# Kernel tuning notes

Hardware: AMD Instinct MI355X
Metric: run time of the kernel (lower is better)

Reference implementation:

```python
import jax, jax.numpy as jnp
import numpy as np

N_NODES = 50000


def gcn_conv(x, src, dst, W, b, n_nodes):
    """PyG-style GCNConv: linear transform, then symmetric-normalized
    aggregation with self-loops added."""
    # add self loops
    loop = jnp.arange(n_nodes, dtype=src.dtype)
    src_l = jnp.concatenate([src, loop])
    dst_l = jnp.concatenate([dst, loop])
    # degree (of dst, including self loops) and symmetric norm
    deg = jax.ops.segment_sum(jnp.ones_like(dst_l, dtype=x.dtype), dst_l,
                              num_segments=n_nodes)
    dinv = jnp.where(deg > 0, jax.lax.rsqrt(deg), 0.0)
    norm = dinv[src_l] * dinv[dst_l]  # [E+N]
    h = x @ W  # [N, out]
    msg = norm[:, None] * h[src_l]  # [E+N, out]
    out = jax.ops.segment_sum(msg, dst_l, num_segments=n_nodes)
    return out + b


def setup_inputs() -> dict:
    key = jax.random.key(0)
    k1, k2, k3, k4 = jax.random.split(key, 4)
    x = jax.random.normal(k1, (N_NODES, 512), dtype=jnp.float32)
    edge_index = jax.random.randint(k2, (2, 800000), 0, N_NODES, dtype=jnp.int32)
    W1 = jax.random.normal(k3, (512, 128), dtype=jnp.float32) * (1.0 / np.sqrt(512))
    b1 = jnp.zeros((128,), dtype=jnp.float32)
    W2 = jax.random.normal(k4, (128, 3), dtype=jnp.float32) * (1.0 / np.sqrt(128))
    b2 = jnp.zeros((3,), dtype=jnp.float32)
    return {"x": x, "edge_index": edge_index, "W1": W1, "b1": b1, "W2": W2, "b2": b2}


def reference(x, edge_index, W1, b1, W2, b2):
    src, dst = edge_index[0], edge_index[1]
    n = x.shape[0]
    h = gcn_conv(x, src, dst, W1, b1, n)
    h = jax.nn.relu(h)
    # dropout is identity in eval mode (training=False)
    out = gcn_conv(h, src, dst, W2, b2, n)
    return out
```

## Files before the change

### kernel.cpp

```cpp
#include <hip/hip_runtime.h>
#include <stdint.h>

#define N_NODES 50000
#define N_EDGES 800000
#define F_IN    512
#define F_HID   128
#define F_OUT   3
#define NBLK_SCAN 196
#define GEMM_BLOCKS 782
#define HIST_BLOCKS 3125
#define FILL_BLOCKS 3125
#define SCALE_BLOCKS 3125

typedef __attribute__((ext_vector_type(8))) short short8;
typedef __attribute__((ext_vector_type(4))) float f32x4;

__device__ __forceinline__ unsigned short f2bf(float f) {
  union { float f; unsigned u; } v; v.f = f;
  unsigned r = v.u + 0x7FFFu + ((v.u >> 16) & 1u);
  return (unsigned short)(r >> 16);
}

__device__ __forceinline__ short8 pack8(float4 a, float4 b) {
  short8 r;
  r[0] = (short)f2bf(a.x); r[1] = (short)f2bf(a.y);
  r[2] = (short)f2bf(a.z); r[3] = (short)f2bf(a.w);
  r[4] = (short)f2bf(b.x); r[5] = (short)f2bf(b.y);
  r[6] = (short)f2bf(b.z); r[7] = (short)f2bf(b.w);
  return r;
}

__device__ __forceinline__ unsigned scale2(unsigned u, float dd) {
  float lo = __uint_as_float(u << 16) * dd;
  float hi = __uint_as_float(u & 0xFFFF0000u) * dd;
  return (unsigned)f2bf(lo) | ((unsigned)f2bf(hi) << 16);
}

__device__ __forceinline__ void g2l16(const void* gsrc, void* ldst) {
  __builtin_amdgcn_global_load_lds(
      (const __attribute__((address_space(1))) unsigned int*)gsrc,
      (__attribute__((address_space(3))) unsigned int*)ldst, 16, 0, 0);
}

__global__ __launch_bounds__(256) void k_prep(const float* __restrict__ W1,
                                              unsigned short* __restrict__ W1t,
                                              int* __restrict__ count) {
  int idx = blockIdx.x * 256 + threadIdx.x;
  if (idx < N_NODES) count[idx] = 0;
  if (idx < F_IN * F_HID) {
    int k = idx >> 7;
    int n = idx & 127;
    W1t[n * F_IN + k] = f2bf(W1[idx]);
  }
}

__global__ __launch_bounds__(256) void k_gemm1_hist(const float* __restrict__ x,
                                                    const unsigned short* __restrict__ W1t,
                                                    unsigned short* __restrict__ h1b,
                                                    const int* __restrict__ dst,
                                                    int* __restrict__ count,
                                                    int* __restrict__ rank) {
  __shared__ float4 AsV[1024];
  __shared__ float4 BsV[1024];
  const int t = threadIdx.x;

  if (blockIdx.x >= GEMM_BLOCKS) {
    int e = (blockIdx.x - GEMM_BLOCKS) * 256 + t;
    if (e < N_EDGES) rank[e] = atomicAdd(&count[dst[e]], 1);
    return;
  }

  char* AsB = (char*)AsV;
  char* BsB = (char*)BsV;
  const int lane = t & 63;
  const int wid = t >> 6;
  const int lane15 = lane & 15;
  const int kgrp = (lane >> 4) << 3;
  const int row0 = blockIdx.x * 64;
  const int wrow = wid << 4;

  f32x4 acc[8];
  #pragma unroll
  for (int j = 0; j < 8; ++j) acc[j] = (f32x4)0.0f;

  for (int kt = 0; kt < 8; ++kt) {
    const int k0 = kt << 6;
    #pragma unroll
    for (int r = 0; r < 4; ++r) {
      const int i = (wid << 2) + r;
      const int o = (i << 10) + (lane << 4);
      {
        const int rowA = o >> 8;
        const int cb = (o & 255) ^ ((rowA & 7) << 4);
        int grow = row0 + rowA;
        grow = grow < N_NODES ? grow : N_NODES - 1;
        g2l16((const char*)x + (size_t)grow * 2048 + (k0 << 2) + cb,
              AsB + (i << 10));
      }
      {
        const int nB = o >> 7;
        const int kb = (o & 127) ^ ((nB & 7) << 4);
        g2l16((const char*)W1t + (size_t)nB * 1024 + (k0 << 1) + kb,
              BsB + (i << 10));
      }
    }
    __syncthreads();
    #pragma unroll
    for (int ks = 0; ks < 2; ++ks) {
      const int kk = (ks << 5) + kgrp;
      const int rowL = wrow + lane15;
      const int swA = (rowL & 7) << 4;
      const float4 xa = *reinterpret_cast<const float4*>(AsB + rowL * 256 + (((kk << 2)) ^ swA));
      const float4 xb = *reinterpret_cast<const float4*>(AsB + rowL * 256 + (((kk << 2) + 16) ^ swA));
      const short8 a = pack8(xa, xb);
      #pragma unroll
      for (int nr = 0; nr < 8; ++nr) {
        const int n = (nr << 4) + lane15;
        const short8 b = *reinterpret_cast<const short8*>(BsB + n * 128 + (((kk << 1)) ^ ((n & 7) << 4)));
        acc[nr] = __builtin_amdgcn_mfma_f32_16x16x32_bf16(a, b, acc[nr], 0, 0, 0);
      }
    }
    __syncthreads();
  }

  const int rgrp = (lane >> 4) << 2;
  const int rowb = row0 + wrow + rgrp;
  #pragma unroll
  for (int nr = 0; nr < 8; ++nr) {
    const int col = (nr << 4) + lane15;
    #pragma unroll
    for (int r = 0; r < 4; ++r) {
      const int row = rowb + r;
      if (row < N_NODES)
        h1b[(size_t)row * F_HID + col] = f2bf(acc[nr][r]);
    }
  }
}

__global__ __launch_bounds__(256) void k_scan1(const int* __restrict__ count,
                                               int* __restrict__ local_pre,
                                               int* __restrict__ blocksum) {
  __shared__ int s[256];
  int t = threadIdx.x;
  int i = blockIdx.x * 256 + t;
  int v = (i < N_NODES) ? count[i] : 0;
  s[t] = v;
  __syncthreads();
  #pragma unroll
  for (int off = 1; off < 256; off <<= 1) {
    int u = (t >= off) ? s[t - off] : 0;
    __syncthreads();
    s[t] += u;
    __syncthreads();
  }
  if (i < N_NODES) local_pre[i] = s[t] - v;
  if (t == 255) blocksum[blockIdx.x] = s[255];
}

__global__ __launch_bounds__(256) void k_scan3(const int* __restrict__ count,
                                               const int* __restrict__ local_pre,
                                               const int* __restrict__ blocksum,
                                               int* __restrict__ row_ptr,
                                               float* __restrict__ dinv) {
  __shared__ int s[256];
  __shared__ int blockoff;
  int t = threadIdx.x;
  int v = (t < NBLK_SCAN) ? blocksum[t] : 0;
  s[t] = v;
  __syncthreads();
  #pragma unroll
  for (int off = 1; off < 256; off <<= 1) {
    int u = (t >= off) ? s[t - off] : 0;
    __syncthreads();
    s[t] += u;
    __syncthreads();
  }
  if (t == blockIdx.x) blockoff = s[t] - v;
  __syncthreads();
  int i = blockIdx.x * 256 + t;
  if (i < N_NODES) {
    row_ptr[i] = local_pre[i] + blockoff;
    dinv[i] = rsqrtf((float)(count[i] + 1));
  }
  if (i == 0) row_ptr[N_NODES] = N_EDGES;
}

__global__ __launch_bounds__(256) void k_fill_scale(const int* __restrict__ src,
                                                    const int* __restrict__ dst,
                                                    const int* __restrict__ row_ptr,
                                                    const int* __restrict__ rank,
                                                    int* __restrict__ csr_src,
                                                    const float* __restrict__ dinv,
                                                    unsigned short* __restrict__ h1b) {
  int t = threadIdx.x;
  if (blockIdx.x < FILL_BLOCKS) {
    int e = blockIdx.x * 256 + t;
    if (e < N_EDGES) {
      int pos = row_ptr[dst[e]] + rank[e];
      csr_src[pos] = src[e];
    }
    return;
  }
  int gid = (blockIdx.x - FILL_BLOCKS) * 256 + t;
  int row = gid >> 4;
  float dd = dinv[row];
  uint4* p = reinterpret_cast<uint4*>(h1b) + gid;
  uint4 v = *p;
  v.x = scale2(v.x, dd);
  v.y = scale2(v.y, dd);
  v.z = scale2(v.z, dd);
  v.w = scale2(v.w, dd);
  *p = v;
}

__global__ __launch_bounds__(256) void k_agg1_fused(const int* __restrict__ row_ptr,
                                                    const int* __restrict__ csr_src,
                                                    const float* __restrict__ dinv,
                                                    const unsigned short* __restrict__ h1b,
                                                    const float* __restrict__ b1,
                                                    const float* __restrict__ W2,
                                                    float* __restrict__ t2p) {
  int t = threadIdx.x;
  int lane = t & 63;
  int node = blockIdx.x * 4 + (t >> 6);
  int g = lane >> 5;
  int fl = (lane & 31) << 2;
  float dd = dinv[node];
  f32x4 acc = (f32x4)0.0f;
  if (g == 0) {
    const uint2 sv = *reinterpret_cast<const uint2*>(h1b + (size_t)node * F_HID + fl);
    acc[0] = __uint_as_float(sv.x << 16);
    acc[1] = __uint_as_float(sv.x & 0xFFFF0000u);
    acc[2] = __uint_as_float(sv.y << 16);
    acc[3] = __uint_as_float(sv.y & 0xFFFF0000u);
  }
  int start = row_ptr[node], end = row_ptr[node + 1];
  int i = start + g;
  for (; i + 6 < end; i += 8) {
    int s0 = csr_src[i];
    int s1 = csr_src[i + 2];
    int s2 = csr_src[i + 4];
    int s3 = csr_src[i + 6];
    const uint2 v0 = *reinterpret_cast<const uint2*>(h1b + (size_t)s0 * F_HID + fl);
    const uint2 v1 = *reinterpret_cast<const uint2*>(h1b + (size_t)s1 * F_HID + fl);
    const uint2 v2 = *reinterpret_cast<const uint2*>(h1b + (size_t)s2 * F_HID + fl);
    const uint2 v3 = *reinterpret_cast<const uint2*>(h1b + (size_t)s3 * F_HID + fl);
    acc[0] += __uint_as_float(v0.x << 16);
    acc[1] += __uint_as_float(v0.x & 0xFFFF0000u);
    acc[2] += __uint_as_float(v0.y << 16);
    acc[3] += __uint_as_float(v0.y & 0xFFFF0000u);
    acc[0] += __uint_as_float(v1.x << 16);
    acc[1] += __uint_as_float(v1.x & 0xFFFF0000u);
    acc[2] += __uint_as_float(v1.y << 16);
    acc[3] += __uint_as_float(v1.y & 0xFFFF0000u);
    acc[0] += __uint_as_float(v2.x << 16);
    acc[1] += __uint_as_float(v2.x & 0xFFFF0000u);
    acc[2] += __uint_as_float(v2.y << 16);
    acc[3] += __uint_as_float(v2.y & 0xFFFF0000u);
    acc[0] += __uint_as_float(v3.x << 16);
    acc[1] += __uint_as_float(v3.x & 0xFFFF0000u);
    acc[2] += __uint_as_float(v3.y << 16);
    acc[3] += __uint_as_float(v3.y & 0xFFFF0000u);
  }
  for (; i < end; i += 2) {
    int s = csr_src[i];
    const uint2 v = *reinterpret_cast<const uint2*>(h1b + (size_t)s * F_HID + fl);
    acc[0] += __uint_as_float(v.x << 16);
    acc[1] += __uint_as_float(v.x & 0xFFFF0000u);
    acc[2] += __uint_as_float(v.y << 16);
    acc[3] += __uint_as_float(v.y & 0xFFFF0000u);
  }
  #pragma unroll
  for (int j = 0; j < 4; ++j) {
    float o = __shfl(acc[j], (lane & 31) + 32);
    acc[j] += o;
  }
  const float4 bb = *reinterpret_cast<const float4*>(b1 + fl);
  float v0 = fmaxf(fmaf(dd, acc[0], bb.x), 0.0f);
  float v1 = fmaxf(fmaf(dd, acc[1], bb.y), 0.0f);
  float v2 = fmaxf(fmaf(dd, acc[2], bb.z), 0.0f);
  float v3 = fmaxf(fmaf(dd, acc[3], bb.w), 0.0f);
  const float* w2r = W2 + fl * 3;
  float pr[3];
  #pragma unroll
  for (int c = 0; c < 3; ++c) {
    float p = v0 * w2r[c] + v1 * w2r[3 + c] + v2 * w2r[6 + c] + v3 * w2r[9 + c];
    p += __shfl_down(p, 16);
    p += __shfl_down(p, 8);
    p += __shfl_down(p, 4);
    p += __shfl_down(p, 2);
    p += __shfl_down(p, 1);
    pr[c] = p;
  }
  if (lane == 0) {
    float4 o;
    o.x = dd * pr[0]; o.y = dd * pr[1]; o.z = dd * pr[2]; o.w = 0.0f;
    *reinterpret_cast<float4*>(t2p + (size_t)node * 4) = o;
  }
}

__global__ __launch_bounds__(256) void k_agg2(const int* __restrict__ row_ptr,
                                              const int* __restrict__ csr_src,
                                              const float* __restrict__ dinv,
                                              const float* __restrict__ t2p,
                                              const float* __restrict__ b2,
                                              float* __restrict__ out) {
  int t = threadIdx.x;
  int node = blockIdx.x * 16 + (t >> 4);
  if (node >= N_NODES) return;
  int sl = t & 15;
  float a0 = 0.f, a1 = 0.f, a2 = 0.f;
  int start = row_ptr[node], end = row_ptr[node + 1];
  for (int i = start + sl; i < end; i += 16) {
    int s = csr_src[i];
    const float4 v = *reinterpret_cast<const float4*>(t2p + (size_t)s * 4);
    a0 += v.x; a1 += v.y; a2 += v.z;
  }
  #pragma unroll
  for (int off = 8; off > 0; off >>= 1) {
    a0 += __shfl_down(a0, off);
    a1 += __shfl_down(a1, off);
    a2 += __shfl_down(a2, off);
  }
  if (sl == 0) {
    float dd = dinv[node];
    const float4 sv = *reinterpret_cast<const float4*>(t2p + (size_t)node * 4);
    out[node * 3 + 0] = fmaf(dd, sv.x + a0, b2[0]);
    out[node * 3 + 1] = fmaf(dd, sv.y + a1, b2[1]);
    out[node * 3 + 2] = fmaf(dd, sv.z + a2, b2[2]);
  }
}

extern "C" void kernel_launch(void* const* d_in, const int* in_sizes, int n_in,
                              void* d_out, int out_size, void* d_ws, size_t ws_size,
                              hipStream_t stream) {
  const float* x  = (const float*)d_in[0];
  const int*   ei = (const int*)d_in[1];
  const float* W1 = (const float*)d_in[2];
  const float* b1 = (const float*)d_in[3];
  const float* W2 = (const float*)d_in[4];
  const float* b2 = (const float*)d_in[5];
  const int* src = ei;
  const int* dst = ei + N_EDGES;
  float* out = (float*)d_out;

  char* ws = (char*)d_ws;
  float*          dinv    = (float*)(ws + 0);
  int*            count   = (int*)  (ws + 200704);
  int*            rank    = (int*)  (ws + 401408);
  int*            row_ptr = (int*)  (ws + 3601408);
  int*            csr_src = (int*)  (ws + 3801600);
  unsigned short* W1t     = (unsigned short*)(ws + 7001600);
  float*          t2p     = (float*)(ws + 7132672);
  int*            local_pre = (int*)(ws + 7933440);
  int*            blocksum  = (int*)(ws + 8133440);
  unsigned short* h1b     = (unsigned short*)(ws + 8134656);

  k_prep      <<<256, 256, 0, stream>>>(W1, W1t, count);
  k_gemm1_hist<<<GEMM_BLOCKS + HIST_BLOCKS, 256, 0, stream>>>(x, W1t, h1b, dst, count, rank);
  k_scan1     <<<NBLK_SCAN, 256, 0, stream>>>(count, local_pre, blocksum);
  k_scan3     <<<NBLK_SCAN, 256, 0, stream>>>(count, local_pre, blocksum, row_ptr, dinv);
  k_fill_scale<<<FILL_BLOCKS + SCALE_BLOCKS, 256, 0, stream>>>(src, dst, row_ptr, rank, csr_src, dinv, h1b);
  k_agg1_fused<<<N_NODES / 4, 256, 0, stream>>>(row_ptr, csr_src, dinv, h1b, b1, W2, t2p);
  k_agg2      <<<(N_NODES + 15) / 16, 256, 0, stream>>>(row_ptr, csr_src, dinv, t2p, b2, out);
}
```

Measured before the change: 119.2 us.

## Move GEMM after degree scan and fold dinv scaling into its epilogue

Reorders the pipeline so the histogram runs alongside the W1 transpose, the scans run next, and the layer-1 GEMM runs afterward with the dinv row scaling applied in its epilogue. The CSR fill now shares a launch with the GEMM. This removes the separate read-modify-write pass over h1b. The count zeroing moves to a memset. The histogram no longer overlaps the GEMM, so the critical path changes.

```diff
diff --git a/kernel.cpp b/kernel.cpp
--- a/kernel.cpp
+++ b/kernel.cpp
@@ -7,10 +7,10 @@
 #define F_HID   128
 #define F_OUT   3
 #define NBLK_SCAN 196
+#define PREP_BLOCKS 256
+#define HIST_BLOCKS 3125
 #define GEMM_BLOCKS 782
-#define HIST_BLOCKS 3125
 #define FILL_BLOCKS 3125
-#define SCALE_BLOCKS 3125
 
 typedef __attribute__((ext_vector_type(8))) short short8;
 typedef __attribute__((ext_vector_type(4))) float f32x4;
@@ -30,43 +30,96 @@
   return r;
 }
 
-__device__ __forceinline__ unsigned scale2(unsigned u, float dd) {
-  float lo = __uint_as_float(u << 16) * dd;
-  float hi = __uint_as_float(u & 0xFFFF0000u) * dd;
-  return (unsigned)f2bf(lo) | ((unsigned)f2bf(hi) << 16);
-}
-
 __device__ __forceinline__ void g2l16(const void* gsrc, void* ldst) {
   __builtin_amdgcn_global_load_lds(
       (const __attribute__((address_space(1))) unsigned int*)gsrc,
       (__attribute__((address_space(3))) unsigned int*)ldst, 16, 0, 0);
 }
 
-__global__ __launch_bounds__(256) void k_prep(const float* __restrict__ W1,
-                                              unsigned short* __restrict__ W1t,
-                                              int* __restrict__ count) {
-  int idx = blockIdx.x * 256 + threadIdx.x;
-  if (idx < N_NODES) count[idx] = 0;
-  if (idx < F_IN * F_HID) {
+__global__ __launch_bounds__(256) void k_prep_hist(const float* __restrict__ W1,
+                                                   unsigned short* __restrict__ W1t,
+                                                   const int* __restrict__ dst,
+                                                   int* __restrict__ count,
+                                                   int* __restrict__ rank) {
+  int t = threadIdx.x;
+  if (blockIdx.x < PREP_BLOCKS) {
+    int idx = blockIdx.x * 256 + t;
     int k = idx >> 7;
     int n = idx & 127;
     W1t[n * F_IN + k] = f2bf(W1[idx]);
-  }
-}
-
-__global__ __launch_bounds__(256) void k_gemm1_hist(const float* __restrict__ x,
+    return;
+  }
+  int e = (blockIdx.x - PREP_BLOCKS) * 256 + t;
+  if (e < N_EDGES) rank[e] = atomicAdd(&count[dst[e]], 1);
+}
+
+__global__ __launch_bounds__(256) void k_scan1(const int* __restrict__ count,
+                                               int* __restrict__ local_pre,
+                                               int* __restrict__ blocksum) {
+  __shared__ int s[256];
+  int t = threadIdx.x;
+  int i = blockIdx.x * 256 + t;
+  int v = (i < N_NODES) ? count[i] : 0;
+  s[t] = v;
+  __syncthreads();
+  #pragma unroll
+  for (int off = 1; off < 256; off <<= 1) {
+    int u = (t >= off) ? s[t - off] : 0;
+    __syncthreads();
+    s[t] += u;
+    __syncthreads();
+  }
+  if (i < N_NODES) local_pre[i] = s[t] - v;
+  if (t == 255) blocksum[blockIdx.x] = s[255];
+}
+
+__global__ __launch_bounds__(256) void k_scan3(const int* __restrict__ count,
+                                               const int* __restrict__ local_pre,
+                                               const int* __restrict__ blocksum,
+                                               int* __restrict__ row_ptr,
+                                               float* __restrict__ dinv) {
+  __shared__ int s[256];
+  __shared__ int blockoff;
+  int t = threadIdx.x;
+  int v = (t < NBLK_SCAN) ? blocksum[t] : 0;
+  s[t] = v;
+  __syncthreads();
+  #pragma unroll
+  for (int off = 1; off < 256; off <<= 1) {
+    int u = (t >= off) ? s[t - off] : 0;
+    __syncthreads();
+    s[t] += u;
+    __syncthreads();
+  }
+  if (t == blockIdx.x) blockoff = s[t] - v;
+  __syncthreads();
+  int i = blockIdx.x * 256 + t;
+  if (i < N_NODES) {
+    row_ptr[i] = local_pre[i] + blockoff;
+    dinv[i] = rsqrtf((float)(count[i] + 1));
+  }
+  if (i == 0) row_ptr[N_NODES] = N_EDGES;
+}
+
+__global__ __launch_bounds__(256) void k_gemm1_fill(const float* __restrict__ x,
                                                     const unsigned short* __restrict__ W1t,
+                                                    const float* __restrict__ dinv,
                                                     unsigned short* __restrict__ h1b,
+                                                    const int* __restrict__ src,
                                                     const int* __restrict__ dst,
-                                                    int* __restrict__ count,
-                                                    int* __restrict__ rank) {
+                                                    const int* __restrict__ row_ptr,
+                                                    const int* __restrict__ rank,
+                                                    int* __restrict__ csr_src) {
   __shared__ float4 AsV[1024];
   __shared__ float4 BsV[1024];
   const int t = threadIdx.x;
 
   if (blockIdx.x >= GEMM_BLOCKS) {
     int e = (blockIdx.x - GEMM_BLOCKS) * 256 + t;
-    if (e < N_EDGES) rank[e] = atomicAdd(&count[dst[e]], 1);
+    if (e < N_EDGES) {
+      int pos = row_ptr[dst[e]] + rank[e];
+      csr_src[pos] = src[e];
+    }
     return;
   }
 
@@ -132,85 +185,9 @@
     for (int r = 0; r < 4; ++r) {
       const int row = rowb + r;
       if (row < N_NODES)
-        h1b[(size_t)row * F_HID + col] = f2bf(acc[nr][r]);
+        h1b[(size_t)row * F_HID + col] = f2bf(dinv[row] * acc[nr][r]);
     }
   }
-}
-
-__global__ __launch_bounds__(256) void k_scan1(const int* __restrict__ count,
-                                               int* __restrict__ local_pre,
-                                               int* __restrict__ blocksum) {
-  __shared__ int s[256];
-  int t = threadIdx.x;
-  int i = blockIdx.x * 256 + t;
-  int v = (i < N_NODES) ? count[i] : 0;
-  s[t] = v;
-  __syncthreads();
-  #pragma unroll
-  for (int off = 1; off < 256; off <<= 1) {
-    int u = (t >= off) ? s[t - off] : 0;
-    __syncthreads();
-    s[t] += u;
-    __syncthreads();
-  }
-  if (i < N_NODES) local_pre[i] = s[t] - v;
-  if (t == 255) blocksum[blockIdx.x] = s[255];
-}
-
-__global__ __launch_bounds__(256) void k_scan3(const int* __restrict__ count,
-                                               const int* __restrict__ local_pre,
-                                               const int* __restrict__ blocksum,
-                                               int* __restrict__ row_ptr,
-                                               float* __restrict__ dinv) {
-  __shared__ int s[256];
-  __shared__ int blockoff;
-  int t = threadIdx.x;
-  int v = (t < NBLK_SCAN) ? blocksum[t] : 0;
-  s[t] = v;
-  __syncthreads();
-  #pragma unroll
-  for (int off = 1; off < 256; off <<= 1) {
-    int u = (t >= off) ? s[t - off] : 0;
-    __syncthreads();
-    s[t] += u;
-    __syncthreads();
-  }
-  if (t == blockIdx.x) blockoff = s[t] - v;
-  __syncthreads();
-  int i = blockIdx.x * 256 + t;
-  if (i < N_NODES) {
-    row_ptr[i] = local_pre[i] + blockoff;
-    dinv[i] = rsqrtf((float)(count[i] + 1));
-  }
-  if (i == 0) row_ptr[N_NODES] = N_EDGES;
-}
-
-__global__ __launch_bounds__(256) void k_fill_scale(const int* __restrict__ src,
-                                                    const int* __restrict__ dst,
-                                                    const int* __restrict__ row_ptr,
-                                                    const int* __restrict__ rank,
-                                                    int* __restrict__ csr_src,
-                                                    const float* __restrict__ dinv,
-                                                    unsigned short* __restrict__ h1b) {
-  int t = threadIdx.x;
-  if (blockIdx.x < FILL_BLOCKS) {
-    int e = blockIdx.x * 256 + t;
-    if (e < N_EDGES) {
-      int pos = row_ptr[dst[e]] + rank[e];
-      csr_src[pos] = src[e];
-    }
-    return;
-  }
-  int gid = (blockIdx.x - FILL_BLOCKS) * 256 + t;
-  int row = gid >> 4;
-  float dd = dinv[row];
-  uint4* p = reinterpret_cast<uint4*>(h1b) + gid;
-  uint4 v = *p;
-  v.x = scale2(v.x, dd);
-  v.y = scale2(v.y, dd);
-  v.z = scale2(v.z, dd);
-  v.w = scale2(v.w, dd);
-  *p = v;
 }
 
 __global__ __launch_bounds__(256) void k_agg1_fused(const int* __restrict__ row_ptr,
@@ -356,11 +333,12 @@
   int*            blocksum  = (int*)(ws + 8133440);
   unsigned short* h1b     = (unsigned short*)(ws + 8134656);
 
-  k_prep      <<<256, 256, 0, stream>>>(W1, W1t, count);
-  k_gemm1_hist<<<GEMM_BLOCKS + HIST_BLOCKS, 256, 0, stream>>>(x, W1t, h1b, dst, count, rank);
+  hipMemsetAsync(count, 0, N_NODES * sizeof(int), stream);
+  k_prep_hist <<<PREP_BLOCKS + HIST_BLOCKS, 256, 0, stream>>>(W1, W1t, dst, count, rank);
   k_scan1     <<<NBLK_SCAN, 256, 0, stream>>>(count, local_pre, blocksum);
   k_scan3     <<<NBLK_SCAN, 256, 0, stream>>>(count, local_pre, blocksum, row_ptr, dinv);
-  k_fill_scale<<<FILL_BLOCKS + SCALE_BLOCKS, 256, 0, stream>>>(src, dst, row_ptr, rank, csr_src, dinv, h1b);
+  k_gemm1_fill<<<GEMM_BLOCKS + FILL_BLOCKS, 256, 0, stream>>>(
+      x, W1t, dinv, h1b, src, dst, row_ptr, rank, csr_src);
   k_agg1_fused<<<N_NODES / 4, 256, 0, stream>>>(row_ptr, csr_src, dinv, h1b, b1, W2, t2p);
   k_agg2      <<<(N_NODES + 15) / 16, 256, 0, stream>>>(row_ptr, csr_src, dinv, t2p, b2, out);
 }
```

Result: slower. 127.7 us (+7.1%).
